# Optimization experiments

Measured on AMD Instinct MI355X. Metric: run time of the kernel, lower is better.

The kernel has to match this reference:

```python
import jax, jax.numpy as jnp
import numpy as np

C_IN = 12      # total channels (rgb-noised + hidden)
C_NOISE = 3    # noise-prediction channels
HID = 128      # rule-MLP hidden size
PERC = 48      # perception channels (depthwise, 48/12 = 4 filters per channel)
TDIM = 256     # sinusoidal time-embedding dim


def setup_inputs() -> dict:
    key = jax.random.key(0)
    ks = jax.random.split(key, 12)
    B, H, W = 16, 256, 256
    x = jax.random.normal(ks[0], (B, C_NOISE, H, W), jnp.float32)
    hidden_channels = jax.random.normal(ks[1], (B, C_IN - C_NOISE, H, W), jnp.float32)
    t = jax.random.randint(ks[2], (B,), 0, 1000)
    # depthwise 3x3 perceive conv: torch weight shape [out=48, in/groups=1, 3, 3]
    w_perceive = jax.random.normal(ks[3], (PERC, 1, 3, 3), jnp.float32) * 0.1
    b_perceive = jax.random.normal(ks[4], (PERC,), jnp.float32) * 0.01
    # 1x1 convs of the rule network, stored as [out, in]
    w1 = jax.random.normal(ks[5], (HID, PERC), jnp.float32) * 0.1
    b1 = jax.random.normal(ks[6], (HID,), jnp.float32) * 0.01
    w2 = jax.random.normal(ks[7], (HID, HID), jnp.float32) * 0.05
    b2 = jax.random.normal(ks[8], (HID,), jnp.float32) * 0.01
    # conv3 is zero-initialized in the original; random here for test coverage
    w3 = jax.random.normal(ks[9], (C_IN, HID), jnp.float32) * 0.05
    # time embedding Linear(256 -> c_noise)
    w_time = jax.random.normal(ks[10], (C_NOISE, TDIM), jnp.float32) * 0.1
    b_time = jax.random.normal(ks[11], (C_NOISE,), jnp.float32) * 0.01
    return dict(x=x, hidden_channels=hidden_channels, t=t,
                w_perceive=w_perceive, b_perceive=b_perceive,
                w1=w1, b1=b1, w2=w2, b2=b2, w3=w3,
                w_time=w_time, b_time=b_time)


def _pos_encoding(t, channels):
    # t: [B] int -> [B, channels] sinusoidal embedding (torch repeat-then-scale layout)
    inv_freq = 1.0 / (10000.0 ** (jnp.arange(0, channels, 2, dtype=jnp.float32) / channels))
    ang = t.astype(jnp.float32)[:, None] * inv_freq  # [B, channels//2]
    return jnp.concatenate([jnp.sin(ang), jnp.cos(ang)], axis=-1)


def reference(x, hidden_channels, t, w_perceive, b_perceive, w1, b1, w2, b2, w3, w_time, b_time):
    # concat noised channels with hidden state channels -> [B, 12, H, W]
    xf = jnp.concatenate([x, hidden_channels], axis=1)
    # depthwise 3x3 conv, 'same' padding, groups = C_IN
    perc = jax.lax.conv_general_dilated(
        xf, w_perceive, window_strides=(1, 1), padding='SAME',
        feature_group_count=C_IN,
        dimension_numbers=('NCHW', 'OIHW', 'NCHW')) + b_perceive[None, :, None, None]
    # rule network: three 1x1 convs (pointwise MLP) with ReLUs
    h = jax.nn.relu(jnp.einsum('bchw,oc->bohw', perc, w1) + b1[None, :, None, None])
    h = jax.nn.relu(jnp.einsum('bchw,oc->bohw', h, w2) + b2[None, :, None, None])
    out = jnp.einsum('bchw,oc->bohw', h, w3)  # no bias
    # time embedding: sinusoidal -> SiLU -> Linear -> broadcast over H, W
    pe = _pos_encoding(t, TDIM)                       # [B, 256]
    emb = jax.nn.silu(pe) @ w_time.T + b_time         # [B, 3]
    noise_prediction = out[:, :C_NOISE] + emb[:, :, None, None]
    hidden_out = out[:, C_NOISE:]
    return (hidden_out, noise_prediction)
```

## Files before the change

kernel.cpp:

```cpp
#include <hip/hip_runtime.h>


#define ACT_S 136
#define NOISE_BASE 9437184

#define WSF_OFF 17408
#define WSF_B1 0
#define WSF_B2 128
#define WSF_EMB 256

typedef short bf16x8 __attribute__((ext_vector_type(8)));
typedef float f32x4 __attribute__((ext_vector_type(4)));

__device__ __forceinline__ short f2bf(float f) {
    union { float f; unsigned u; } cv; cv.f = f;
    unsigned r = cv.u + 0x7FFFu + ((cv.u >> 16) & 1u);
    return (short)(r >> 16);
}
__device__ __forceinline__ unsigned pk2bf(float f0, float f1) {
    union { float f; unsigned u; } a, b; a.f = f0; b.f = f1;
    return __builtin_amdgcn_perm(b.u + 0x8000u, a.u + 0x8000u, 0x07060302u);
}

__device__ __forceinline__ int permch64(int f) {
    return (f & ~63) + 16 * ((f >> 2) & 3) + 4 * ((f >> 4) & 3) + (f & 3);
}

__global__ void prep_emb_kernel(const float* __restrict__ wpg, const float* __restrict__ bpg,
                                const float* __restrict__ w1g, const float* __restrict__ b1g,
                                const float* __restrict__ w2g, const float* __restrict__ b2g,
                                const float* __restrict__ w3g,
                                const int* __restrict__ t,
                                const float* __restrict__ wt, const float* __restrict__ bt,
                                short* __restrict__ wsb, float* __restrict__ wsf)
{
    const int bid = blockIdx.x, tid = threadIdx.x;
    if (bid < 64) {
        int i = bid * 256 + tid;
        int f = i >> 7, kk = i & 127;
        int o = permch64(f);
        int qq = kk >> 5, r = kk & 31;
        float v = 0.f;
        if (r < 30 && (r % 10) < 9) {
            int c3 = r / 10, k = r % 10;
            int ic = 3 * qq + c3;
            #pragma unroll
            for (int j = 0; j < 4; ++j)
                v += w1g[o * 48 + 4 * ic + j] * wpg[(4 * ic + j) * 9 + k];
        }
        wsb[i] = f2bf(v);
        return;
    }
    if (bid < 128) {
        int i = (bid - 64) * 256 + tid;
        int f = i >> 7, col = i & 127;
        wsb[16384 + i] = f2bf(w2g[permch64(f) * 128 + col]);
        return;
    }
    if (bid == 128) {
        for (int j = tid; j < 2048; j += 256)
            wsb[32768 + j] = (j < 1536) ? f2bf(w3g[j]) : (short)0;
        return;
    }
    if (bid == 129) {
        if (tid < 128) {
            float s = b1g[tid];
            #pragma unroll 4
            for (int c = 0; c < 48; ++c) s += w1g[tid * 48 + c] * bpg[c];
            wsf[WSF_B1 + tid] = s;
        } else {
            wsf[WSF_B2 + (tid - 128)] = b2g[tid - 128];
        }
        return;
    }
    int b = bid - 130;
    int lane = threadIdx.x;
    if (lane >= 64) return;
    float tv = (float)t[b];
    float s0 = 0.f, s1 = 0.f, s2 = 0.f;
    const float LOG1E4 = 9.210340371976184f;
    #pragma unroll
    for (int ii = 0; ii < 2; ++ii) {
        int i = lane + ii * 64;
        float invf = __expf(-LOG1E4 * (float)i * (1.0f / 128.0f));
        float ang = tv * invf;
        float sn = sinf(ang), cs = cosf(ang);
        float ss = sn / (1.0f + __expf(-sn));
        float sc = cs / (1.0f + __expf(-cs));
        s0 += ss * wt[0 * 256 + i] + sc * wt[0 * 256 + i + 128];
        s1 += ss * wt[1 * 256 + i] + sc * wt[1 * 256 + i + 128];
        s2 += ss * wt[2 * 256 + i] + sc * wt[2 * 256 + i + 128];
    }
    #pragma unroll
    for (int off = 32; off; off >>= 1) {
        s0 += __shfl_down(s0, off);
        s1 += __shfl_down(s1, off);
        s2 += __shfl_down(s2, off);
    }
    if (lane == 0) {
        wsf[WSF_EMB + b * 3 + 0] = s0 + bt[0];
        wsf[WSF_EMB + b * 3 + 1] = s1 + bt[1];
        wsf[WSF_EMB + b * 3 + 2] = s2 + bt[2];
    }
}

__global__ __launch_bounds__(256, 2) void canet_main(
    const float* __restrict__ xg,
    const float* __restrict__ hg,
    const short* __restrict__ wsb,
    const float* __restrict__ wsf,
    float* __restrict__ outg)
{
    __shared__ __align__(16) short bufA[64 * ACT_S];
    __shared__ __align__(16) short h1S[64 * ACT_S];
    __shared__ __align__(16) short w3_s[16 * 128];
    __shared__ __align__(16) float bias_s[256];

    const int tid = threadIdx.x;
    const int b = blockIdx.x >> 8;
    const int y = blockIdx.x & 255;

    bias_s[tid] = wsf[WSF_B1 + tid];
    for (int i = tid; i < 2048; i += 256) {
        int row = i >> 7, col = i & 127;
        w3_s[(row << 7) + (col ^ ((row & 7) << 3))] = wsb[32768 + i];
    }

    const int wv = tid >> 6;
    const int lane = tid & 63;
    const int m = lane & 15;
    const int q = lane >> 4;
    const int wc = wv >> 1;
    const int wp = wv & 1;

    bf16x8 w1f[4][4], w2f[4][4];
    #pragma unroll
    for (int jt = 0; jt < 4; ++jt) {
        int n = wc * 64 + jt * 16 + m;
        #pragma unroll
        for (int ks = 0; ks < 4; ++ks) {
            w1f[jt][ks] = *(const bf16x8*)(wsb + n * 128 + ks * 32 + q * 8);
            w2f[jt][ks] = *(const bf16x8*)(wsb + 16384 + n * 128 + ks * 32 + q * 8);
        }
    }
    const float embv = (m < 3) ? wsf[WSF_EMB + b * 3 + m] : 0.0f;

    const float* src3[3];
    #pragma unroll
    for (int i3 = 0; i3 < 3; ++i3) {
        int ic = 3 * q + i3;
        src3[i3] = (ic < 3) ? (xg + (((size_t)b * 3 + ic) << 16))
                            : (hg + (((size_t)b * 9 + (ic - 3)) << 16));
    }
    int yoff[3]; bool yokk[3];
    #pragma unroll
    for (int ky = 0; ky < 3; ++ky) {
        int yy = y + ky - 1;
        yokk[ky] = (yy >= 0) && (yy < 256);
        yoff[ky] = (yokk[ky] ? yy : y) * 256;
    }

    auto load_taps = [&](float (&tp)[27], int pxl) {
        const int xm1 = pxl - (pxl > 0);
        const int xp1 = pxl + (pxl < 255);
        #pragma unroll
        for (int i3 = 0; i3 < 3; ++i3) {
            #pragma unroll
            for (int ky = 0; ky < 3; ++ky) {
                const float* rp = src3[i3] + yoff[ky];
                tp[i3 * 9 + ky * 3 + 0] = rp[xm1];
                tp[i3 * 9 + ky * 3 + 1] = rp[pxl];
                tp[i3 * 9 + ky * 3 + 2] = rp[xp1];
            }
        }
    };

    const int w3sw = (m & 7) << 3;

    float tp[27];
    load_taps(tp, wv * 16 + m);

    __syncthreads();

    for (int it = 0; it < 4; ++it) {
        const int x0 = it * 64;
        const int px = x0 + wv * 16 + m;

        {
            const bool okl = (px > 0), okr = (px < 255);
            short* prow = bufA + (wv * 16 + m) * ACT_S + 32 * q;
            unsigned rr[16];
            rr[15] = 0u;
            #pragma unroll
            for (int i3 = 0; i3 < 3; ++i3) {
                float tm[9];
                #pragma unroll
                for (int ky = 0; ky < 3; ++ky) {
                    int o = i3 * 9 + ky * 3;
                    tm[ky * 3 + 0] = (yokk[ky] && okl) ? tp[o + 0] : 0.0f;
                    tm[ky * 3 + 1] = yokk[ky] ? tp[o + 1] : 0.0f;
                    tm[ky * 3 + 2] = (yokk[ky] && okr) ? tp[o + 2] : 0.0f;
                }
                rr[5 * i3 + 0] = pk2bf(tm[0], tm[1]);
                rr[5 * i3 + 1] = pk2bf(tm[2], tm[3]);
                rr[5 * i3 + 2] = pk2bf(tm[4], tm[5]);
                rr[5 * i3 + 3] = pk2bf(tm[6], tm[7]);
                rr[5 * i3 + 4] = pk2bf(tm[8], 0.0f);
            }
            #pragma unroll
            for (int w = 0; w < 4; ++w) {
                uint4 v; v.x = rr[4*w]; v.y = rr[4*w+1]; v.z = rr[4*w+2]; v.w = rr[4*w+3];
                *(uint4*)(prow + 8 * w) = v;
            }
        }
        __syncthreads();

        if (it < 3) load_taps(tp, px + 64);

        #pragma unroll
        for (int nt = 0; nt < 2; ++nt) {
            const int prow = (wp * 32 + nt * 16 + m) * ACT_S;
            f32x4 d0 = *(const f32x4*)(bias_s + wc * 64 + 16 * q + 0);
            f32x4 d1 = *(const f32x4*)(bias_s + wc * 64 + 16 * q + 4);
            f32x4 d2 = *(const f32x4*)(bias_s + wc * 64 + 16 * q + 8);
            f32x4 d3 = *(const f32x4*)(bias_s + wc * 64 + 16 * q + 12);
            #pragma unroll
            for (int ks = 0; ks < 4; ++ks) {
                bf16x8 p = *(const bf16x8*)(bufA + prow + ks * 32 + q * 8);
                d0 = __builtin_amdgcn_mfma_f32_16x16x32_bf16(w1f[0][ks], p, d0, 0, 0, 0);
                d1 = __builtin_amdgcn_mfma_f32_16x16x32_bf16(w1f[1][ks], p, d1, 0, 0, 0);
                d2 = __builtin_amdgcn_mfma_f32_16x16x32_bf16(w1f[2][ks], p, d2, 0, 0, 0);
                d3 = __builtin_amdgcn_mfma_f32_16x16x32_bf16(w1f[3][ks], p, d3, 0, 0, 0);
            }
            short* drow = h1S + prow + wc * 64 + 16 * q;
            uint4 A, B;
            A.x = pk2bf(fmaxf(d0[0], 0.f), fmaxf(d0[1], 0.f));
            A.y = pk2bf(fmaxf(d0[2], 0.f), fmaxf(d0[3], 0.f));
            A.z = pk2bf(fmaxf(d1[0], 0.f), fmaxf(d1[1], 0.f));
            A.w = pk2bf(fmaxf(d1[2], 0.f), fmaxf(d1[3], 0.f));
            B.x = pk2bf(fmaxf(d2[0], 0.f), fmaxf(d2[1], 0.f));
            B.y = pk2bf(fmaxf(d2[2], 0.f), fmaxf(d2[3], 0.f));
            B.z = pk2bf(fmaxf(d3[0], 0.f), fmaxf(d3[1], 0.f));
            B.w = pk2bf(fmaxf(d3[2], 0.f), fmaxf(d3[3], 0.f));
            *(uint4*)drow = A;
            *(uint4*)(drow + 8) = B;
        }
        __syncthreads();

        #pragma unroll
        for (int nt = 0; nt < 2; ++nt) {
            const int prow = (wp * 32 + nt * 16 + m) * ACT_S;
            f32x4 d0 = *(const f32x4*)(bias_s + 128 + wc * 64 + 16 * q + 0);
            f32x4 d1 = *(const f32x4*)(bias_s + 128 + wc * 64 + 16 * q + 4);
            f32x4 d2 = *(const f32x4*)(bias_s + 128 + wc * 64 + 16 * q + 8);
            f32x4 d3 = *(const f32x4*)(bias_s + 128 + wc * 64 + 16 * q + 12);
            #pragma unroll
            for (int ks = 0; ks < 4; ++ks) {
                bf16x8 a = *(const bf16x8*)(h1S + prow + ks * 32 + q * 8);
                d0 = __builtin_amdgcn_mfma_f32_16x16x32_bf16(w2f[0][ks], a, d0, 0, 0, 0);
                d1 = __builtin_amdgcn_mfma_f32_16x16x32_bf16(w2f[1][ks], a, d1, 0, 0, 0);
                d2 = __builtin_amdgcn_mfma_f32_16x16x32_bf16(w2f[2][ks], a, d2, 0, 0, 0);
                d3 = __builtin_amdgcn_mfma_f32_16x16x32_bf16(w2f[3][ks], a, d3, 0, 0, 0);
            }
            short* drow = bufA + prow + wc * 64 + 16 * q;
            uint4 A, B;
            A.x = pk2bf(fmaxf(d0[0], 0.f), fmaxf(d0[1], 0.f));
            A.y = pk2bf(fmaxf(d0[2], 0.f), fmaxf(d0[3], 0.f));
            A.z = pk2bf(fmaxf(d1[0], 0.f), fmaxf(d1[1], 0.f));
            A.w = pk2bf(fmaxf(d1[2], 0.f), fmaxf(d1[3], 0.f));
            B.x = pk2bf(fmaxf(d2[0], 0.f), fmaxf(d2[1], 0.f));
            B.y = pk2bf(fmaxf(d2[2], 0.f), fmaxf(d2[3], 0.f));
            B.z = pk2bf(fmaxf(d3[0], 0.f), fmaxf(d3[1], 0.f));
            B.w = pk2bf(fmaxf(d3[2], 0.f), fmaxf(d3[3], 0.f));
            *(uint4*)drow = A;
            *(uint4*)(drow + 8) = B;
        }
        __syncthreads();

        {
            f32x4 acc = {0.f, 0.f, 0.f, 0.f};
            #pragma unroll
            for (int ks = 0; ks < 4; ++ks) {
                bf16x8 a = *(const bf16x8*)(bufA + (wv * 16 + m) * ACT_S + ks * 32 + q * 8);
                bf16x8 w3k = *(const bf16x8*)(w3_s + (m << 7) + ((ks * 32 + q * 8) ^ w3sw));
                acc = __builtin_amdgcn_mfma_f32_16x16x32_bf16(a, w3k, acc, 0, 0, 0);
            }
            if (m < 12) {
                int xx0 = x0 + wv * 16 + q * 4;
                size_t idx;
                if (m < 3) {
                    idx = (size_t)NOISE_BASE + (((size_t)b * 3 + m) << 16) + (size_t)y * 256 + xx0;
                } else {
                    idx = (((size_t)b * 9 + (m - 3)) << 16) + (size_t)y * 256 + xx0;
                }
                f32x4 vst = {acc[0] + embv, acc[1] + embv, acc[2] + embv, acc[3] + embv};
                *(f32x4*)(outg + idx) = vst;
            }
        }
        __syncthreads();
    }
}

extern "C" void kernel_launch(void* const* d_in, const int* in_sizes, int n_in,
                              void* d_out, int out_size, void* d_ws, size_t ws_size,
                              hipStream_t stream) {
    const float* xg  = (const float*)d_in[0];
    const float* hg  = (const float*)d_in[1];
    const int*   tg  = (const int*)  d_in[2];
    const float* wpg = (const float*)d_in[3];
    const float* bpg = (const float*)d_in[4];
    const float* w1g = (const float*)d_in[5];
    const float* b1g = (const float*)d_in[6];
    const float* w2g = (const float*)d_in[7];
    const float* b2g = (const float*)d_in[8];
    const float* w3g = (const float*)d_in[9];
    const float* wtg = (const float*)d_in[10];
    const float* btg = (const float*)d_in[11];
    float* outg = (float*)d_out;
    short* wsb  = (short*)d_ws;
    float* wsf  = (float*)d_ws + WSF_OFF;

    prep_emb_kernel<<<146, 256, 0, stream>>>(wpg, bpg, w1g, b1g, w2g, b2g, w3g,
                                             tg, wtg, btg, wsb, wsf);
    canet_main<<<4096, 256, 0, stream>>>(xg, hg, wsb, wsf, outg);
}
```

Before: 246.1 us.

## Split layer-1 GEMM across waves by output channels to cut register use

Layer-1 work is repartitioned so that each wave computes 32 output channels for all 64 pixels, instead of 64 channels for 32 pixels. This halves the per-wave w1 register fragments, and the weight channel permutation is changed to match. Launch bounds are raised to three blocks per SM to exploit the lower register pressure. In exchange, each wave now reads the full activation tile from LDS, so LDS read traffic for layer 1 doubles.

```diff
diff --git a/kernel.cpp b/kernel.cpp
--- a/kernel.cpp
+++ b/kernel.cpp
@@ -22,6 +22,9 @@
     return __builtin_amdgcn_perm(b.u + 0x8000u, a.u + 0x8000u, 0x07060302u);
 }
 
+__device__ __forceinline__ int permch(int f) {
+    return (f & ~31) + 8 * ((f & 15) >> 2) + 4 * ((f >> 4) & 1) + (f & 3);
+}
 __device__ __forceinline__ int permch64(int f) {
     return (f & ~63) + 16 * ((f >> 2) & 3) + 4 * ((f >> 4) & 3) + (f & 3);
 }
@@ -38,7 +41,7 @@
     if (bid < 64) {
         int i = bid * 256 + tid;
         int f = i >> 7, kk = i & 127;
-        int o = permch64(f);
+        int o = permch(f);
         int qq = kk >> 5, r = kk & 31;
         float v = 0.f;
         if (r < 30 && (r % 10) < 9) {
@@ -104,7 +107,7 @@
     }
 }
 
-__global__ __launch_bounds__(256, 2) void canet_main(
+__global__ __launch_bounds__(256, 3) void canet_main(
     const float* __restrict__ xg,
     const float* __restrict__ hg,
     const short* __restrict__ wsb,
@@ -133,15 +136,20 @@
     const int wc = wv >> 1;
     const int wp = wv & 1;
 
-    bf16x8 w1f[4][4], w2f[4][4];
+    bf16x8 w1f[2][4], w2f[4][4];
+    #pragma unroll
+    for (int j = 0; j < 2; ++j) {
+        int n = wv * 32 + j * 16 + m;
+        #pragma unroll
+        for (int ks = 0; ks < 4; ++ks)
+            w1f[j][ks] = *(const bf16x8*)(wsb + n * 128 + ks * 32 + q * 8);
+    }
     #pragma unroll
     for (int jt = 0; jt < 4; ++jt) {
         int n = wc * 64 + jt * 16 + m;
         #pragma unroll
-        for (int ks = 0; ks < 4; ++ks) {
-            w1f[jt][ks] = *(const bf16x8*)(wsb + n * 128 + ks * 32 + q * 8);
+        for (int ks = 0; ks < 4; ++ks)
             w2f[jt][ks] = *(const bf16x8*)(wsb + 16384 + n * 128 + ks * 32 + q * 8);
-        }
     }
     const float embv = (m < 3) ? wsf[WSF_EMB + b * 3 + m] : 0.0f;
 
@@ -218,32 +226,22 @@
         if (it < 3) load_taps(tp, px + 64);
 
         #pragma unroll
-        for (int nt = 0; nt < 2; ++nt) {
-            const int prow = (wp * 32 + nt * 16 + m) * ACT_S;
-            f32x4 d0 = *(const f32x4*)(bias_s + wc * 64 + 16 * q + 0);
-            f32x4 d1 = *(const f32x4*)(bias_s + wc * 64 + 16 * q + 4);
-            f32x4 d2 = *(const f32x4*)(bias_s + wc * 64 + 16 * q + 8);
-            f32x4 d3 = *(const f32x4*)(bias_s + wc * 64 + 16 * q + 12);
+        for (int nt = 0; nt < 4; ++nt) {
+            f32x4 c0 = *(const f32x4*)(bias_s + wv * 32 + 8 * q);
+            f32x4 c1 = *(const f32x4*)(bias_s + wv * 32 + 8 * q + 4);
             #pragma unroll
             for (int ks = 0; ks < 4; ++ks) {
-                bf16x8 p = *(const bf16x8*)(bufA + prow + ks * 32 + q * 8);
-                d0 = __builtin_amdgcn_mfma_f32_16x16x32_bf16(w1f[0][ks], p, d0, 0, 0, 0);
-                d1 = __builtin_amdgcn_mfma_f32_16x16x32_bf16(w1f[1][ks], p, d1, 0, 0, 0);
-                d2 = __builtin_amdgcn_mfma_f32_16x16x32_bf16(w1f[2][ks], p, d2, 0, 0, 0);
-                d3 = __builtin_amdgcn_mfma_f32_16x16x32_bf16(w1f[3][ks], p, d3, 0, 0, 0);
-            }
-            short* drow = h1S + prow + wc * 64 + 16 * q;
-            uint4 A, B;
-            A.x = pk2bf(fmaxf(d0[0], 0.f), fmaxf(d0[1], 0.f));
-            A.y = pk2bf(fmaxf(d0[2], 0.f), fmaxf(d0[3], 0.f));
-            A.z = pk2bf(fmaxf(d1[0], 0.f), fmaxf(d1[1], 0.f));
-            A.w = pk2bf(fmaxf(d1[2], 0.f), fmaxf(d1[3], 0.f));
-            B.x = pk2bf(fmaxf(d2[0], 0.f), fmaxf(d2[1], 0.f));
-            B.y = pk2bf(fmaxf(d2[2], 0.f), fmaxf(d2[3], 0.f));
-            B.z = pk2bf(fmaxf(d3[0], 0.f), fmaxf(d3[1], 0.f));
-            B.w = pk2bf(fmaxf(d3[2], 0.f), fmaxf(d3[3], 0.f));
-            *(uint4*)drow = A;
-            *(uint4*)(drow + 8) = B;
+                bf16x8 p = *(const bf16x8*)(bufA + (nt * 16 + m) * ACT_S + ks * 32 + q * 8);
+                c0 = __builtin_amdgcn_mfma_f32_16x16x32_bf16(w1f[0][ks], p, c0, 0, 0, 0);
+                c1 = __builtin_amdgcn_mfma_f32_16x16x32_bf16(w1f[1][ks], p, c1, 0, 0, 0);
+            }
+            short* drow = h1S + (nt * 16 + m) * ACT_S + wv * 32 + 8 * q;
+            uint4 pk4;
+            pk4.x = pk2bf(fmaxf(c0[0], 0.f), fmaxf(c0[1], 0.f));
+            pk4.y = pk2bf(fmaxf(c0[2], 0.f), fmaxf(c0[3], 0.f));
+            pk4.z = pk2bf(fmaxf(c1[0], 0.f), fmaxf(c1[1], 0.f));
+            pk4.w = pk2bf(fmaxf(c1[2], 0.f), fmaxf(c1[3], 0.f));
+            *(uint4*)drow = pk4;
         }
         __syncthreads();
 
```

Result: slower. 502.2 us (+104.0%).
